# Performance work log

Hardware: AMD Instinct MI355X
Metric: run time of the kernel (lower is better)

The kernel has to match this reference:

```python
import jax, jax.numpy as jnp
import numpy as np

D_MODEL = 256; N_HEADS = 8; HEAD_DIM = 32; N_LEVELS = 4; N_POINTS = 4; N_LAYERS = 3; D_FFN = 1024
SHAPES = np.array([[76, 76], [38, 38], [19, 19], [10, 10]], dtype=np.int64)
S_TOTAL = int((SHAPES[:, 0] * SHAPES[:, 1]).sum())  # 7681


def setup_inputs():
    key = jax.random.key(0)
    ks = jax.random.split(key, 12)
    B = 1; C = D_MODEL; M = N_HEADS; Lv = N_LEVELS; P = N_POINTS; L = N_LAYERS; s = 0.02
    starts = np.concatenate([[0], np.cumsum(SHAPES[:, 0] * SHAPES[:, 1])[:-1]]).astype(np.int64)
    inp = {
        "src": jax.random.normal(ks[0], (B, S_TOTAL, C), jnp.float32),
        "pos": jax.random.normal(ks[1], (B, S_TOTAL, C), jnp.float32),
        "valid_ratios": jnp.ones((B, Lv, 2), jnp.float32),
        "spatial_shapes": jnp.asarray(SHAPES),
        "level_start_index": jnp.asarray(starts),
        "padding_mask": jnp.zeros((B, S_TOTAL), bool),
        "W_off": jax.random.normal(ks[2], (L, C, M * Lv * P * 2), jnp.float32) * s,
        "b_off": jax.random.normal(ks[3], (L, M * Lv * P * 2), jnp.float32) * s,
        "W_attn": jax.random.normal(ks[4], (L, C, M * Lv * P), jnp.float32) * s,
        "b_attn": jax.random.normal(ks[5], (L, M * Lv * P), jnp.float32) * s,
        "W_val": jax.random.normal(ks[6], (L, C, C), jnp.float32) * s,
        "b_val": jnp.zeros((L, C), jnp.float32),
        "W_out": jax.random.normal(ks[7], (L, C, C), jnp.float32) * s,
        "b_out": jnp.zeros((L, C), jnp.float32),
        "ln1_g": jnp.ones((L, C), jnp.float32),
        "ln1_b": jnp.zeros((L, C), jnp.float32),
        "W_ff1": jax.random.normal(ks[8], (L, C, D_FFN), jnp.float32) * s,
        "b_ff1": jnp.zeros((L, D_FFN), jnp.float32),
        "W_ff2": jax.random.normal(ks[9], (L, D_FFN, C), jnp.float32) * s,
        "b_ff2": jnp.zeros((L, C), jnp.float32),
        "ln2_g": jnp.ones((L, C), jnp.float32),
        "ln2_b": jnp.zeros((L, C), jnp.float32),
    }
    return inp


def _ln(x, g, b):
    mu = x.mean(-1, keepdims=True)
    var = ((x - mu) ** 2).mean(-1, keepdims=True)
    return (x - mu) * jax.lax.rsqrt(var + 1e-5) * g + b


def _gather(v, idx):
    # v: [B, HW, M, D], idx: [B, S, M, P] -> [B, S, M, P, D], head-specific gather
    B, S, M, P = idx.shape
    def one(vb, ib):
        i2 = ib.transpose(0, 2, 1).reshape(S * P, M, 1)
        o = jnp.take_along_axis(vb, i2, axis=0)  # [S*P, M, D]
        return o.reshape(S, P, M, -1).transpose(0, 2, 1, 3)
    return jax.vmap(one)(v, idx)


def _msda(query, src, mask, ref, shapes, starts, Wo, bo, Wa, ba, Wv, bv, Wout, bout):
    # Multi-scale deformable attention (Deformable-DETR), grid_sample align_corners=False + zero padding
    B, S, C = src.shape
    M, Lv, P, D = N_HEADS, N_LEVELS, N_POINTS, HEAD_DIM
    value = src @ Wv + bv
    value = jnp.where(mask[..., None], 0.0, value).reshape(B, S, M, D)
    off = (query @ Wo + bo).reshape(B, S, M, Lv, P, 2)
    aw = jax.nn.softmax((query @ Wa + ba).reshape(B, S, M, Lv * P), -1).reshape(B, S, M, Lv, P)
    norm = jnp.asarray(shapes[:, ::-1].copy(), jnp.float32)  # (W, H) per level
    loc = ref[:, :, None, :, None, :] + off / norm[None, None, None, :, None, :]  # [B,S,M,Lv,P,2]
    out = jnp.zeros((B, S, M, D), query.dtype)
    for lvl in range(Lv):
        H = int(shapes[lvl, 0]); W = int(shapes[lvl, 1]); st = int(starts[lvl])
        v = value[:, st:st + H * W]  # [B, H*W, M, D]
        l = loc[:, :, :, lvl]  # [B, S, M, P, 2]
        x = l[..., 0] * W - 0.5
        y = l[..., 1] * H - 0.5
        x0 = jnp.floor(x); y0 = jnp.floor(y)
        dx = x - x0; dy = y - y0
        samp = jnp.zeros((B, S, M, P, D), query.dtype)
        for yy, xx, w in ((y0, x0, (1 - dy) * (1 - dx)), (y0, x0 + 1, (1 - dy) * dx),
                          (y0 + 1, x0, dy * (1 - dx)), (y0 + 1, x0 + 1, dy * dx)):
            valid = (xx >= 0) & (xx < W) & (yy >= 0) & (yy < H)
            xi = jnp.clip(xx, 0, W - 1).astype(jnp.int32)
            yi = jnp.clip(yy, 0, H - 1).astype(jnp.int32)
            g = _gather(v, yi * W + xi)
            samp = samp + (w * valid)[..., None] * g
        out = out + (aw[:, :, :, lvl, :, None] * samp).sum(3)
    return out.reshape(B, S, C) @ Wout + bout


def _ref_points(vr, shapes):
    refs = []
    for lvl in range(shapes.shape[0]):
        H = int(shapes[lvl, 0]); W = int(shapes[lvl, 1])
        ry, rx = np.meshgrid(np.linspace(0.5, H - 0.5, H, dtype=np.float32),
                             np.linspace(0.5, W - 0.5, W, dtype=np.float32), indexing="ij")
        rxj = jnp.asarray(rx.reshape(-1))[None] / (vr[:, None, lvl, 0] * W)
        ryj = jnp.asarray(ry.reshape(-1))[None] / (vr[:, None, lvl, 1] * H)
        refs.append(jnp.stack([rxj, ryj], -1))
    ref = jnp.concatenate(refs, 1)  # [B, S, 2]
    return ref[:, :, None] * vr[:, None]  # [B, S, Lv, 2]


def _encoder(src, pos, valid_ratios, shapes, starts, mask, params):
    (W_off, b_off, W_attn, b_attn, W_val, b_val, W_out, b_out,
     ln1_g, ln1_b, W_ff1, b_ff1, W_ff2, b_ff2, ln2_g, ln2_b) = params
    ref = _ref_points(valid_ratios, shapes)
    out = src
    for l in range(N_LAYERS):
        q = out + pos  # with_pos_embed
        a = _msda(q, out, mask, ref, shapes, starts, W_off[l], b_off[l], W_attn[l], b_attn[l],
                  W_val[l], b_val[l], W_out[l], b_out[l])
        out = _ln(out + a, ln1_g[l], ln1_b[l])
        f = jax.nn.relu(out @ W_ff1[l] + b_ff1[l]) @ W_ff2[l] + b_ff2[l]
        out = _ln(out + f, ln2_g[l], ln2_b[l])
    return out


def reference(src, pos, valid_ratios, spatial_shapes, level_start_index, padding_mask,
              W_off, b_off, W_attn, b_attn, W_val, b_val, W_out, b_out,
              ln1_g, ln1_b, W_ff1, b_ff1, W_ff2, b_ff2, ln2_g, ln2_b):
    shapes = np.asarray(spatial_shapes)
    starts = np.asarray(level_start_index)
    params = (W_off, b_off, W_attn, b_attn, W_val, b_val, W_out, b_out,
              ln1_g, ln1_b, W_ff1, b_ff1, W_ff2, b_ff2, ln2_g, ln2_b)
    return _encoder(src, pos, valid_ratios, shapes, starts, padding_mask, params)
```

## Files before the change

kernel.cpp:

```cpp
#include <hip/hip_runtime.h>
#include <hip/hip_bf16.h>
#include <math.h>

#define S_TOTAL 7681

typedef __attribute__((ext_vector_type(8))) short bf16x8;
typedef __attribute__((ext_vector_type(4))) float f32x4;

__device__ __forceinline__ short f2b(float x) {
    union { float f; unsigned u; } v; v.f = x;
    unsigned r = v.u + 0x7FFFu + ((v.u >> 16) & 1u);
    return (short)(r >> 16);
}
__device__ __forceinline__ float b2f(unsigned short u) {
    union { unsigned u; float f; } t; t.u = ((unsigned)u) << 16; return t.f;
}

#define BM 128
#define BN 64
#define BK 32
#define KP 40

#define N4_TOT 491584
__global__ __launch_bounds__(256) void prologue_kernel(
    const float* __restrict__ s0, const float* __restrict__ s1,
    const float* __restrict__ s2, const float* __restrict__ s3,
    const float* __restrict__ s4, const float* __restrict__ s5,
    short* __restrict__ d0, short* __restrict__ d1, short* __restrict__ d2,
    short* __restrict__ d3, short* __restrict__ d4, short* __restrict__ d5,
    const float4* __restrict__ src, const float4* __restrict__ pos,
    float4* __restrict__ o, ushort4* __restrict__ xb, ushort4* __restrict__ qb)
{
    int b = blockIdx.x;
    if (b >= 2208) {
        int i = (b - 2208) * 256 + threadIdx.x;
        if (i < N4_TOT) {
            float4 v = src[i], p = pos[i];
            o[i] = v;
            ushort4 h, hq;
            h.x = (unsigned short)f2b(v.x); h.y = (unsigned short)f2b(v.y);
            h.z = (unsigned short)f2b(v.z); h.w = (unsigned short)f2b(v.w);
            hq.x = (unsigned short)f2b(v.x + p.x); hq.y = (unsigned short)f2b(v.y + p.y);
            hq.z = (unsigned short)f2b(v.z + p.z); hq.w = (unsigned short)f2b(v.w + p.w);
            xb[i] = h;
            qb[i] = hq;
        }
        return;
    }
    const int z = b / 736;
    int t = b - z * 736;
    const float* src_w; short* dst; int K, N, lt;
    if (t < 64)       { src_w = s0 + (size_t)z * 65536;  dst = d0 + (size_t)z * 65536;  K = 256;  N = 256;  lt = t; }
    else if (t < 128) { src_w = s1 + (size_t)z * 65536;  dst = d1 + (size_t)z * 98304;  K = 256;  N = 256;  lt = t - 64; }
    else if (t < 160) { src_w = s2 + (size_t)z * 32768;  dst = d2 + (size_t)z * 98304;  K = 256;  N = 128;  lt = t - 128; }
    else if (t < 224) { src_w = s3 + (size_t)z * 65536;  dst = d3 + (size_t)z * 65536;  K = 256;  N = 256;  lt = t - 160; }
    else if (t < 480) { src_w = s4 + (size_t)z * 262144; dst = d4 + (size_t)z * 262144; K = 256;  N = 1024; lt = t - 224; }
    else              { src_w = s5 + (size_t)z * 262144; dst = d5 + (size_t)z * 262144; K = 1024; N = 256;  lt = t - 480; }
    const int ntx = N >> 5;
    const int tk = (lt / ntx) << 5, tn = (lt % ntx) << 5;
    __shared__ float tile[32][33];
    const int cx = threadIdx.x & 31, cy = threadIdx.x >> 5;
    #pragma unroll
    for (int i = 0; i < 32; i += 8)
        tile[cy + i][cx] = src_w[(size_t)(tk + cy + i) * N + tn + cx];
    __syncthreads();
    #pragma unroll
    for (int i = 0; i < 32; i += 8)
        dst[(size_t)(tn + cy + i) * K + tk + cx] = f2b(tile[cx][cy + i]);
}

__global__ __launch_bounds__(256) void gemm_va_kernel(
    const short* __restrict__ xb, const short* __restrict__ qb,
    const short* __restrict__ Wt_val, const short* __restrict__ Wt_oa,
    const float* __restrict__ b_val, const float* __restrict__ b_off,
    const float* __restrict__ b_attn,
    short* __restrict__ value_bf, float* __restrict__ offbuf, int M)
{
    const int grp = (blockIdx.y >= 4);
    const short* A  = grp ? qb : xb;
    const short* Wt = grp ? Wt_oa : Wt_val;
    const int colBase = (grp ? (blockIdx.y - 4) : blockIdx.y) * BN;
    const int K = 256;

    __shared__ __align__(16) short As[BM * KP];
    __shared__ __align__(16) short Bs[BN * KP];
    const int tid = threadIdx.x;
    const int lane = tid & 63;
    const int wave = tid >> 6;
    const int rowBase = blockIdx.x * BM;

    const int ar = tid >> 1;
    const int ak = (tid & 1) * 16;
    const int br = tid >> 2;
    const int bk = (tid & 3) * 8;

    const int frow = lane & 15;
    const int fko  = (lane >> 4) * 8;
    const int wm = wave * 32;

    f32x4 acc[2][4] = {};

    const int aRow = rowBase + ar;
    const bool aOk = aRow < M;
    const short* Ap = A + (size_t)aRow * K + ak;
    const short* Bp = Wt + (size_t)(colBase + br) * K + bk;

    bf16x8 a0 = {}, a1 = {}, b0 = {};
    if (aOk) { a0 = *(const bf16x8*)Ap; a1 = *(const bf16x8*)(Ap + 8); }
    b0 = *(const bf16x8*)Bp;

    for (int k0 = 0; k0 < K; k0 += BK) {
        *(bf16x8*)&As[ar * KP + ak]     = a0;
        *(bf16x8*)&As[ar * KP + ak + 8] = a1;
        *(bf16x8*)&Bs[br * KP + bk]     = b0;
        __syncthreads();

        const int kn = k0 + BK;
        if (kn < K) {
            if (aOk) { a0 = *(const bf16x8*)(Ap + kn); a1 = *(const bf16x8*)(Ap + kn + 8); }
            b0 = *(const bf16x8*)(Bp + kn);
        }

        bf16x8 af0 = *(const bf16x8*)&As[(wm + frow) * KP + fko];
        bf16x8 af1 = *(const bf16x8*)&As[(wm + 16 + frow) * KP + fko];
        #pragma unroll
        for (int j = 0; j < 4; ++j) {
            bf16x8 bfj = *(const bf16x8*)&Bs[(j * 16 + frow) * KP + fko];
            acc[0][j] = __builtin_amdgcn_mfma_f32_16x16x32_bf16(af0, bfj, acc[0][j], 0, 0, 0);
            acc[1][j] = __builtin_amdgcn_mfma_f32_16x16x32_bf16(af1, bfj, acc[1][j], 0, 0, 0);
        }
        __syncthreads();
    }

    const int erow = (lane >> 4) * 4;
    const int ecol = lane & 15;
    #pragma unroll
    for (int mi = 0; mi < 2; ++mi) {
        #pragma unroll
        for (int j = 0; j < 4; ++j) {
            int col = colBase + j * 16 + ecol;
            float bias = grp ? (col < 256 ? b_off[col] : b_attn[col - 256]) : b_val[col];
            #pragma unroll
            for (int r = 0; r < 4; ++r) {
                int row = rowBase + wm + mi * 16 + erow + r;
                if (row < M) {
                    float v = acc[mi][j][r] + bias;
                    if (grp) offbuf[(size_t)row * 384 + col] = v;
                    else     value_bf[(size_t)row * 256 + col] = f2b(v);
                }
            }
        }
    }
}

__global__ __launch_bounds__(256) void gemm_ff1_kernel(
    const short* __restrict__ A, const short* __restrict__ Wt,
    const float* __restrict__ bias, short* __restrict__ Cv,
    int M, int N, int K)
{
    __shared__ __align__(16) short As[BM * KP];
    __shared__ __align__(16) short Bs[BN * KP];
    const int tid = threadIdx.x;
    const int lane = tid & 63;
    const int wave = tid >> 6;
    const int rowBase = blockIdx.x * BM;
    const int colBase = blockIdx.y * BN;

    const int ar = tid >> 1;
    const int ak = (tid & 1) * 16;
    const int br = tid >> 2;
    const int bk = (tid & 3) * 8;

    const int frow = lane & 15;
    const int fko  = (lane >> 4) * 8;
    const int wm = wave * 32;

    f32x4 acc[2][4] = {};

    const int aRow = rowBase + ar;
    const bool aOk = aRow < M;
    const short* Ap = A + (size_t)aRow * K + ak;
    const short* Bp = Wt + (size_t)(colBase + br) * K + bk;

    bf16x8 a0 = {}, a1 = {}, b0 = {};
    if (aOk) { a0 = *(const bf16x8*)Ap; a1 = *(const bf16x8*)(Ap + 8); }
    b0 = *(const bf16x8*)Bp;

    for (int k0 = 0; k0 < K; k0 += BK) {
        *(bf16x8*)&As[ar * KP + ak]     = a0;
        *(bf16x8*)&As[ar * KP + ak + 8] = a1;
        *(bf16x8*)&Bs[br * KP + bk]     = b0;
        __syncthreads();

        const int kn = k0 + BK;
        if (kn < K) {
            if (aOk) { a0 = *(const bf16x8*)(Ap + kn); a1 = *(const bf16x8*)(Ap + kn + 8); }
            b0 = *(const bf16x8*)(Bp + kn);
        }

        bf16x8 af0 = *(const bf16x8*)&As[(wm + frow) * KP + fko];
        bf16x8 af1 = *(const bf16x8*)&As[(wm + 16 + frow) * KP + fko];
        #pragma unroll
        for (int j = 0; j < 4; ++j) {
            bf16x8 bfj = *(const bf16x8*)&Bs[(j * 16 + frow) * KP + fko];
            acc[0][j] = __builtin_amdgcn_mfma_f32_16x16x32_bf16(af0, bfj, acc[0][j], 0, 0, 0);
            acc[1][j] = __builtin_amdgcn_mfma_f32_16x16x32_bf16(af1, bfj, acc[1][j], 0, 0, 0);
        }
        __syncthreads();
    }

    const int erow = (lane >> 4) * 4;
    const int ecol = lane & 15;
    #pragma unroll
    for (int mi = 0; mi < 2; ++mi) {
        #pragma unroll
        for (int j = 0; j < 4; ++j) {
            #pragma unroll
            for (int r = 0; r < 4; ++r) {
                int row = rowBase + wm + mi * 16 + erow + r;
                if (row < M) {
                    int col = colBase + j * 16 + ecol;
                    float v = fmaxf(acc[mi][j][r] + bias[col], 0.f);
                    Cv[(size_t)row * N + col] = f2b(v);
                }
            }
        }
    }
}

__global__ __launch_bounds__(256) void msda_outln_kernel(
    const short* __restrict__ value, const float* __restrict__ offb,
    const short* __restrict__ Wt_out, const float* __restrict__ bias,
    const float* __restrict__ g, const float* __restrict__ bln,
    float* __restrict__ out, short* __restrict__ xb, int M)
{
    __shared__ __align__(16) char scratch[36864];
    __shared__ __align__(16) short mt[16 * 264];
    __shared__ float rsum[16][4], rsq[16][4], smu[16], srs[16];
    float*   soff = (float*)scratch;
    ushort4* sIdx = (ushort4*)(scratch + 12288);
    float4*  sWgt = (float4*)(scratch + 20480);
    short*   Bs   = (short*)scratch;

    const int bid = blockIdx.x;
    const int sb = (bid < 480) ? ((bid & 7) * 60 + (bid >> 3)) : 480;
    const int q0 = sb * 16;
    const int tid = threadIdx.x;
    const int lane = tid & 63;
    const int wave = tid >> 6;

    for (int t = 0; t < 2; ++t) {
        const int qs = q0 + t * 8;
        {
            const float4* src4 = (const float4*)offb;
            float4* soff4 = (float4*)soff;
            #pragma unroll
            for (int i = tid; i < 768; i += 256) {
                int qi = i / 96, j = i - qi * 96;
                int q = min(qs + qi, S_TOTAL - 1);
                soff4[qi * 96 + j] = src4[(size_t)q * 96 + j];
            }
        }
        __syncthreads();

        if (tid < 64) {
            const int qi = tid >> 3, m = tid & 7;
            float* lg = &soff[qi * 384 + 256 + m * 16];
            float mx = -1e30f;
            #pragma unroll
            for (int k = 0; k < 16; ++k) mx = fmaxf(mx, lg[k]);
            float e[16], sum = 0.f;
            #pragma unroll
            for (int k = 0; k < 16; ++k) { e[k] = expf(lg[k] - mx); sum += e[k]; }
            float inv = 1.f / sum;
            #pragma unroll
            for (int k = 0; k < 16; ++k) lg[k] = e[k] * inv;
        }
        __syncthreads();

        #pragma unroll
        for (int it = tid; it < 1024; it += 256) {
            const int qi = it >> 7, i = it & 127;
            const int lvl = (i >> 2) & 3;
            const int q = min(qs + qi, S_TOTAL - 1);

            float refx, refy;
            if (q < 5776)      { int u = q;        int r = u / 76, c = u % 76; refx = (c + 0.5f) / 76.f; refy = (r + 0.5f) / 76.f; }
            else if (q < 7220) { int u = q - 5776; int r = u / 38, c = u % 38; refx = (c + 0.5f) / 38.f; refy = (r + 0.5f) / 38.f; }
            else if (q < 7581) { int u = q - 7220; int r = u / 19, c = u % 19; refx = (c + 0.5f) / 19.f; refy = (r + 0.5f) / 19.f; }
            else               { int u = q - 7581; int r = u / 10, c = u % 10; refx = (c + 0.5f) / 10.f; refy = (r + 0.5f) / 10.f; }

            const int LVL_HW[4] = {76, 38, 19, 10};
            const int LVL_ST[4] = {0, 5776, 7220, 7581};
            const int W = LVL_HW[lvl];
            const float fW = (float)W;

            float ox = soff[qi * 384 + i * 2];
            float oy = soff[qi * 384 + i * 2 + 1];
            float aw = soff[qi * 384 + 256 + i];

            float x = refx * fW + ox - 0.5f;
            float y = refy * fW + oy - 0.5f;
            float x0f = floorf(x), y0f = floorf(y);
            int x0 = (int)x0f, y0 = (int)y0f;
            float dx = x - x0f, dy = y - y0f;

            bool vx0 = (x0 >= 0) & (x0 < W);
            bool vx1 = (x0 >= -1) & (x0 < W - 1);
            bool vy0 = (y0 >= 0) & (y0 < W);
            bool vy1 = (y0 >= -1) & (y0 < W - 1);
            int xc0 = min(max(x0, 0), W - 1), xc1 = min(max(x0 + 1, 0), W - 1);
            int yc0 = min(max(y0, 0), W - 1), yc1 = min(max(y0 + 1, 0), W - 1);
            int base = LVL_ST[lvl];
            ushort4 id;
            id.x = (unsigned short)(base + yc0 * W + xc0);
            id.y = (unsigned short)(base + yc0 * W + xc1);
            id.z = (unsigned short)(base + yc1 * W + xc0);
            id.w = (unsigned short)(base + yc1 * W + xc1);
            float4 w4;
            w4.x = (vy0 && vx0) ? (1.f - dy) * (1.f - dx) * aw : 0.f;
            w4.y = (vy0 && vx1) ? (1.f - dy) * dx * aw : 0.f;
            w4.z = (vy1 && vx0) ? dy * (1.f - dx) * aw : 0.f;
            w4.w = (vy1 && vx1) ? dy * dx * aw : 0.f;
            sIdx[it] = id;
            sWgt[it] = w4;
        }
        __syncthreads();

        {
            const int qi = wave * 2 + ((lane >> 5) & 1);
            const int l32 = lane & 31;
            const int h = l32 >> 2, dg = l32 & 3;
            const short* vcol = value + h * 32 + dg * 8;
            const int itb = qi * 128 + (h << 4);

            float a[8] = {};
            #pragma unroll
            for (int pt = 0; pt < 16; ++pt) {
                const ushort4 id = sIdx[itb + pt];
                const float4 w = sWgt[itb + pt];
                bf16x8 v0 = *(const bf16x8*)(vcol + ((size_t)id.x << 8));
                bf16x8 v1 = *(const bf16x8*)(vcol + ((size_t)id.y << 8));
                bf16x8 v2 = *(const bf16x8*)(vcol + ((size_t)id.z << 8));
                bf16x8 v3 = *(const bf16x8*)(vcol + ((size_t)id.w << 8));
                #pragma unroll
                for (int e = 0; e < 8; ++e)
                    a[e] += w.x * b2f((unsigned short)v0[e]) + w.y * b2f((unsigned short)v1[e])
                          + w.z * b2f((unsigned short)v2[e]) + w.w * b2f((unsigned short)v3[e]);
            }
            bf16x8 o;
            #pragma unroll
            for (int e = 0; e < 8; ++e) o[e] = f2b(a[e]);
            *(bf16x8*)&mt[(t * 8 + qi) * 264 + h * 32 + dg * 8] = o;
        }
        __syncthreads();
    }

    const int frow = lane & 15;
    const int fko  = (lane >> 4) * 8;

    f32x4 acc[4] = {};
    const short* Bp = Wt_out + (size_t)tid * 256;
    bf16x8 w0 = *(const bf16x8*)(Bp);      bf16x8 w1 = *(const bf16x8*)(Bp + 8);
    bf16x8 w2 = *(const bf16x8*)(Bp + 16); bf16x8 w3 = *(const bf16x8*)(Bp + 24);

    for (int k0 = 0; k0 < 256; k0 += BK) {
        *(bf16x8*)&Bs[tid * KP + 0]  = w0;
        *(bf16x8*)&Bs[tid * KP + 8]  = w1;
        *(bf16x8*)&Bs[tid * KP + 16] = w2;
        *(bf16x8*)&Bs[tid * KP + 24] = w3;
        __syncthreads();

        const int kn = k0 + BK;
        if (kn < 256) {
            w0 = *(const bf16x8*)(Bp + kn);      w1 = *(const bf16x8*)(Bp + kn + 8);
            w2 = *(const bf16x8*)(Bp + kn + 16); w3 = *(const bf16x8*)(Bp + kn + 24);
        }

        bf16x8 af = *(const bf16x8*)&mt[frow * 264 + k0 + fko];
        #pragma unroll
        for (int j = 0; j < 4; ++j) {
            bf16x8 bfj = *(const bf16x8*)&Bs[(wave * 64 + j * 16 + frow) * KP + fko];
            acc[j] = __builtin_amdgcn_mfma_f32_16x16x32_bf16(af, bfj, acc[j], 0, 0, 0);
        }
        __syncthreads();
    }

    const int erow = (lane >> 4) * 4;
    const int ecol = lane & 15;
    float x[4][4];
    #pragma unroll
    for (int j = 0; j < 4; ++j)
        #pragma unroll
        for (int r = 0; r < 4; ++r) {
            int row = q0 + erow + r;
            int col = wave * 64 + j * 16 + ecol;
            float res = (row < M) ? out[(size_t)row * 256 + col] : 0.f;
            x[j][r] = acc[j][r] + bias[col] + res;
        }

    #pragma unroll
    for (int r = 0; r < 4; ++r) {
        float s1 = x[0][r] + x[1][r] + x[2][r] + x[3][r];
        float s2 = x[0][r]*x[0][r] + x[1][r]*x[1][r] + x[2][r]*x[2][r] + x[3][r]*x[3][r];
        #pragma unroll
        for (int o = 1; o < 16; o <<= 1) {
            s1 += __shfl_xor(s1, o);
            s2 += __shfl_xor(s2, o);
        }
        if ((lane & 15) == 0) {
            rsum[erow + r][wave] = s1;
            rsq [erow + r][wave] = s2;
        }
    }
    __syncthreads();
    if (tid < 16) {
        float S1 = rsum[tid][0] + rsum[tid][1] + rsum[tid][2] + rsum[tid][3];
        float S2 = rsq[tid][0] + rsq[tid][1] + rsq[tid][2] + rsq[tid][3];
        float mu = S1 * (1.f / 256.f);
        smu[tid] = mu;
        srs[tid] = rsqrtf(S2 * (1.f / 256.f) - mu * mu + 1e-5f);
    }
    __syncthreads();

    #pragma unroll
    for (int r = 0; r < 4; ++r) {
        int lrow = erow + r;
        int row = q0 + lrow;
        if (row >= M) continue;
        float mu = smu[lrow], rs = srs[lrow];
        #pragma unroll
        for (int j = 0; j < 4; ++j) {
            int col = wave * 64 + j * 16 + ecol;
            float y = (x[j][r] - mu) * rs * g[col] + bln[col];
            out[(size_t)row * 256 + col] = y;
            xb[(size_t)row * 256 + col] = f2b(y);
        }
    }
}

template<int WRITEQ>
__global__ __launch_bounds__(256) void gemm_ln16_kernel(
    const short* __restrict__ A, const short* __restrict__ Wt,
    const float* __restrict__ bias, const float* __restrict__ g,
    const float* __restrict__ bln, const float* __restrict__ pos,
    float* __restrict__ out, short* __restrict__ xb, short* __restrict__ qb,
    int M, int K)
{
    __shared__ __align__(16) short As[16 * KP];
    __shared__ __align__(16) short Bs[256 * KP];
    __shared__ float rsum[16][4], rsq[16][4], smu[16], srs[16];

    const int tid = threadIdx.x;
    const int lane = tid & 63;
    const int wave = tid >> 6;
    const int rowBase = blockIdx.x * 16;

    const int frow = lane & 15;
    const int fko  = (lane >> 4) * 8;

    f32x4 acc[4] = {};

    const int ar = tid >> 1;
    const int ak = (tid & 1) * 16;
    const int aRow = rowBase + ar;
    const bool aOk = (tid < 32) && (aRow < M);
    const short* Ap = A + (size_t)aRow * K + ak;
    const short* Bp = Wt + (size_t)tid * K;

    bf16x8 a0 = {}, a1 = {};
    if (aOk) { a0 = *(const bf16x8*)Ap; a1 = *(const bf16x8*)(Ap + 8); }
    bf16x8 w0 = *(const bf16x8*)(Bp);      bf16x8 w1 = *(const bf16x8*)(Bp + 8);
    bf16x8 w2 = *(const bf16x8*)(Bp + 16); bf16x8 w3 = *(const bf16x8*)(Bp + 24);

    for (int k0 = 0; k0 < K; k0 += BK) {
        if (tid < 32) {
            *(bf16x8*)&As[ar * KP + ak]     = a0;
            *(bf16x8*)&As[ar * KP + ak + 8] = a1;
        }
        *(bf16x8*)&Bs[tid * KP + 0]  = w0;
        *(bf16x8*)&Bs[tid * KP + 8]  = w1;
        *(bf16x8*)&Bs[tid * KP + 16] = w2;
        *(bf16x8*)&Bs[tid * KP + 24] = w3;
        __syncthreads();

        const int kn = k0 + BK;
        if (kn < K) {
            if (aOk) { a0 = *(const bf16x8*)(Ap + kn); a1 = *(const bf16x8*)(Ap + kn + 8); }
            w0 = *(const bf16x8*)(Bp + kn);      w1 = *(const bf16x8*)(Bp + kn + 8);
            w2 = *(const bf16x8*)(Bp + kn + 16); w3 = *(const bf16x8*)(Bp + kn + 24);
        }

        bf16x8 af = *(const bf16x8*)&As[frow * KP + fko];
        #pragma unroll
        for (int j = 0; j < 4; ++j) {
            bf16x8 bfj = *(const bf16x8*)&Bs[(wave * 64 + j * 16 + frow) * KP + fko];
            acc[j] = __builtin_amdgcn_mfma_f32_16x16x32_bf16(af, bfj, acc[j], 0, 0, 0);
        }
        __syncthreads();
    }

    const int erow = (lane >> 4) * 4;
    const int ecol = lane & 15;
    float x[4][4];
    #pragma unroll
    for (int j = 0; j < 4; ++j)
        #pragma unroll
        for (int r = 0; r < 4; ++r) {
            int row = rowBase + erow + r;
            int col = wave * 64 + j * 16 + ecol;
            float res = (row < M) ? out[(size_t)row * 256 + col] : 0.f;
            x[j][r] = acc[j][r] + bias[col] + res;
        }

    #pragma unroll
    for (int r = 0; r < 4; ++r) {
        float s1 = x[0][r] + x[1][r] + x[2][r] + x[3][r];
        float s2 = x[0][r]*x[0][r] + x[1][r]*x[1][r] + x[2][r]*x[2][r] + x[3][r]*x[3][r];
        #pragma unroll
        for (int o = 1; o < 16; o <<= 1) {
            s1 += __shfl_xor(s1, o);
            s2 += __shfl_xor(s2, o);
        }
        if ((lane & 15) == 0) {
            rsum[erow + r][wave] = s1;
            rsq [erow + r][wave] = s2;
        }
    }
    __syncthreads();
    if (tid < 16) {
        float S1 = rsum[tid][0] + rsum[tid][1] + rsum[tid][2] + rsum[tid][3];
        float S2 = rsq[tid][0] + rsq[tid][1] + rsq[tid][2] + rsq[tid][3];
        float mu = S1 * (1.f / 256.f);
        smu[tid] = mu;
        srs[tid] = rsqrtf(S2 * (1.f / 256.f) - mu * mu + 1e-5f);
    }
    __syncthreads();

    #pragma unroll
    for (int r = 0; r < 4; ++r) {
        int lrow = erow + r;
        int row = rowBase + lrow;
        if (row >= M) continue;
        float mu = smu[lrow], rs = srs[lrow];
        #pragma unroll
        for (int j = 0; j < 4; ++j) {
            int col = wave * 64 + j * 16 + ecol;
            float y = (x[j][r] - mu) * rs * g[col] + bln[col];
            out[(size_t)row * 256 + col] = y;
            xb[(size_t)row * 256 + col] = f2b(y);
            if (WRITEQ)
                qb[(size_t)row * 256 + col] = f2b(y + pos[(size_t)row * 256 + col]);
        }
    }
}

extern "C" void kernel_launch(void* const* d_in, const int* in_sizes, int n_in,
                              void* d_out, int out_size, void* d_ws, size_t ws_size,
                              hipStream_t stream) {
    const float* src    = (const float*)d_in[0];
    const float* pos    = (const float*)d_in[1];
    const float* W_off  = (const float*)d_in[6];
    const float* b_off  = (const float*)d_in[7];
    const float* W_attn = (const float*)d_in[8];
    const float* b_attn = (const float*)d_in[9];
    const float* W_val  = (const float*)d_in[10];
    const float* b_val  = (const float*)d_in[11];
    const float* W_out  = (const float*)d_in[12];
    const float* b_out  = (const float*)d_in[13];
    const float* ln1_g  = (const float*)d_in[14];
    const float* ln1_b  = (const float*)d_in[15];
    const float* W_ff1  = (const float*)d_in[16];
    const float* b_ff1  = (const float*)d_in[17];
    const float* W_ff2  = (const float*)d_in[18];
    const float* b_ff2  = (const float*)d_in[19];
    const float* ln2_g  = (const float*)d_in[20];
    const float* ln2_b  = (const float*)d_in[21];

    const size_t S = S_TOTAL;
    float* out = (float*)d_out;

    short* wt = (short*)d_ws;
    short* Wt_val = wt;
    short* Wt_oa  = wt + 196608;
    short* Wt_out = wt + 491520;
    short* Wt_ff1 = wt + 688128;
    short* Wt_ff2 = wt + 1474560;
    float* fbase  = (float*)d_ws + 1131648;
    short* xb       = (short*)fbase;
    short* qb       = (short*)(fbase + 128 * S);
    short* value_bf = (short*)(fbase + 256 * S);
    float* offb     = fbase + 384 * S;
    short* hid      = (short*)(fbase + 256 * S);

    prologue_kernel<<<4129, 256, 0, stream>>>(
        W_val, W_off, W_attn, W_out, W_ff1, W_ff2,
        Wt_val, Wt_oa, Wt_oa + 65536, Wt_out, Wt_ff1, Wt_ff2,
        (const float4*)src, (const float4*)pos,
        (float4*)out, (ushort4*)xb, (ushort4*)qb);

    const int MB = (S_TOTAL + BM - 1) / BM;
    const int LB = (S_TOTAL + 15) / 16;

    for (int l = 0; l < 3; ++l) {
        gemm_va_kernel<<<dim3(MB, 10), 256, 0, stream>>>(
            xb, qb, Wt_val + (size_t)l * 65536, Wt_oa + (size_t)l * 98304,
            b_val + (size_t)l * 256, b_off + (size_t)l * 256, b_attn + (size_t)l * 128,
            value_bf, offb, S_TOTAL);
        msda_outln_kernel<<<LB, 256, 0, stream>>>(
            value_bf, offb, Wt_out + (size_t)l * 65536, b_out + (size_t)l * 256,
            ln1_g + (size_t)l * 256, ln1_b + (size_t)l * 256,
            out, xb, S_TOTAL);
        gemm_ff1_kernel<<<dim3(MB, 16), 256, 0, stream>>>(
            xb, Wt_ff1 + (size_t)l * 262144, b_ff1 + (size_t)l * 1024, hid,
            S_TOTAL, 1024, 256);
        gemm_ln16_kernel<1><<<LB, 256, 0, stream>>>(
            hid, Wt_ff2 + (size_t)l * 262144, b_ff2 + (size_t)l * 256,
            ln2_g + (size_t)l * 256, ln2_b + (size_t)l * 256, pos,
            out, xb, qb, S_TOTAL, 1024);
    }
}
```

Measured before the change: 449.1 us.

## Split MSDA sampling from output projection and reuse the LN GEMM kernel

The fused MSDA+out-proj+LayerNorm kernel is split into two. A standalone sampling kernel processes 8 queries per block over 968 blocks and writes bf16 results to a new global buffer. The existing gemm_ln16 kernel (WRITEQ=0) then does the output projection, residual add and LayerNorm. This is meant to raise block count and occupancy for the gather-heavy sampling stage and to use the tuned GEMM path. In exchange it adds a kernel launch and a global round trip of the sampled activations.

```diff
diff --git a/kernel.cpp b/kernel.cpp
--- a/kernel.cpp
+++ b/kernel.cpp
@@ -228,215 +228,129 @@
     }
 }
 
-__global__ __launch_bounds__(256) void msda_outln_kernel(
+__global__ __launch_bounds__(256) void msda_kernel(
     const short* __restrict__ value, const float* __restrict__ offb,
-    const short* __restrict__ Wt_out, const float* __restrict__ bias,
-    const float* __restrict__ g, const float* __restrict__ bln,
-    float* __restrict__ out, short* __restrict__ xb, int M)
+    short* __restrict__ msdab)
 {
-    __shared__ __align__(16) char scratch[36864];
-    __shared__ __align__(16) short mt[16 * 264];
-    __shared__ float rsum[16][4], rsq[16][4], smu[16], srs[16];
+    __shared__ __align__(16) char scratch[24576];
     float*   soff = (float*)scratch;
-    ushort4* sIdx = (ushort4*)(scratch + 12288);
-    float4*  sWgt = (float4*)(scratch + 20480);
-    short*   Bs   = (short*)scratch;
+    ushort4* sIdx = (ushort4*)scratch;
+    float4*  sWgt = (float4*)(scratch + 8192);
 
     const int bid = blockIdx.x;
-    const int sb = (bid < 480) ? ((bid & 7) * 60 + (bid >> 3)) : 480;
-    const int q0 = sb * 16;
+    const int sb = (bid & 7) * 121 + (bid >> 3);
+    const int q0 = sb * 8;
+    if (q0 >= S_TOTAL) return;
     const int tid = threadIdx.x;
+
+    {
+        const float4* src4 = (const float4*)offb;
+        float4* soff4 = (float4*)soff;
+        #pragma unroll
+        for (int i = tid; i < 768; i += 256) {
+            int qi = i / 96, j = i - qi * 96;
+            int q = min(q0 + qi, S_TOTAL - 1);
+            soff4[qi * 96 + j] = src4[(size_t)q * 96 + j];
+        }
+    }
+    __syncthreads();
+
+    if (tid < 64) {
+        const int qi = tid >> 3, m = tid & 7;
+        float* lg = &soff[qi * 384 + 256 + m * 16];
+        float mx = -1e30f;
+        #pragma unroll
+        for (int k = 0; k < 16; ++k) mx = fmaxf(mx, lg[k]);
+        float e[16], sum = 0.f;
+        #pragma unroll
+        for (int k = 0; k < 16; ++k) { e[k] = expf(lg[k] - mx); sum += e[k]; }
+        float inv = 1.f / sum;
+        #pragma unroll
+        for (int k = 0; k < 16; ++k) lg[k] = e[k] * inv;
+    }
+    __syncthreads();
+
+    ushort4 rid[4];
+    float4  rw[4];
+    #pragma unroll
+    for (int k = 0; k < 4; ++k) {
+        const int it = tid + k * 256;
+        const int qi = it >> 7, i = it & 127;
+        const int lvl = (i >> 2) & 3;
+        const int q = min(q0 + qi, S_TOTAL - 1);
+
+        float refx, refy;
+        if (q < 5776)      { int u = q;        int r = u / 76, c = u % 76; refx = (c + 0.5f) / 76.f; refy = (r + 0.5f) / 76.f; }
+        else if (q < 7220) { int u = q - 5776; int r = u / 38, c = u % 38; refx = (c + 0.5f) / 38.f; refy = (r + 0.5f) / 38.f; }
+        else if (q < 7581) { int u = q - 7220; int r = u / 19, c = u % 19; refx = (c + 0.5f) / 19.f; refy = (r + 0.5f) / 19.f; }
+        else               { int u = q - 7581; int r = u / 10, c = u % 10; refx = (c + 0.5f) / 10.f; refy = (r + 0.5f) / 10.f; }
+
+        const int LVL_HW[4] = {76, 38, 19, 10};
+        const int LVL_ST[4] = {0, 5776, 7220, 7581};
+        const int W = LVL_HW[lvl];
+        const float fW = (float)W;
+
+        float ox = soff[qi * 384 + i * 2];
+        float oy = soff[qi * 384 + i * 2 + 1];
+        float aw = soff[qi * 384 + 256 + i];
+
+        float x = refx * fW + ox - 0.5f;
+        float y = refy * fW + oy - 0.5f;
+        float x0f = floorf(x), y0f = floorf(y);
+        int x0 = (int)x0f, y0 = (int)y0f;
+        float dx = x - x0f, dy = y - y0f;
+
+        bool vx0 = (x0 >= 0) & (x0 < W);
+        bool vx1 = (x0 >= -1) & (x0 < W - 1);
+        bool vy0 = (y0 >= 0) & (y0 < W);
+        bool vy1 = (y0 >= -1) & (y0 < W - 1);
+        int xc0 = min(max(x0, 0), W - 1), xc1 = min(max(x0 + 1, 0), W - 1);
+        int yc0 = min(max(y0, 0), W - 1), yc1 = min(max(y0 + 1, 0), W - 1);
+        int base = LVL_ST[lvl];
+        rid[k].x = (unsigned short)(base + yc0 * W + xc0);
+        rid[k].y = (unsigned short)(base + yc0 * W + xc1);
+        rid[k].z = (unsigned short)(base + yc1 * W + xc0);
+        rid[k].w = (unsigned short)(base + yc1 * W + xc1);
+        rw[k].x = (vy0 && vx0) ? (1.f - dy) * (1.f - dx) * aw : 0.f;
+        rw[k].y = (vy0 && vx1) ? (1.f - dy) * dx * aw : 0.f;
+        rw[k].z = (vy1 && vx0) ? dy * (1.f - dx) * aw : 0.f;
+        rw[k].w = (vy1 && vx1) ? dy * dx * aw : 0.f;
+    }
+    __syncthreads();
+    #pragma unroll
+    for (int k = 0; k < 4; ++k) {
+        sIdx[tid + k * 256] = rid[k];
+        sWgt[tid + k * 256] = rw[k];
+    }
+    __syncthreads();
+
     const int lane = tid & 63;
-    const int wave = tid >> 6;
-
-    for (int t = 0; t < 2; ++t) {
-        const int qs = q0 + t * 8;
-        {
-            const float4* src4 = (const float4*)offb;
-            float4* soff4 = (float4*)soff;
-            #pragma unroll
-            for (int i = tid; i < 768; i += 256) {
-                int qi = i / 96, j = i - qi * 96;
-                int q = min(qs + qi, S_TOTAL - 1);
-                soff4[qi * 96 + j] = src4[(size_t)q * 96 + j];
-            }
-        }
-        __syncthreads();
-
-        if (tid < 64) {
-            const int qi = tid >> 3, m = tid & 7;
-            float* lg = &soff[qi * 384 + 256 + m * 16];
-            float mx = -1e30f;
-            #pragma unroll
-            for (int k = 0; k < 16; ++k) mx = fmaxf(mx, lg[k]);
-            float e[16], sum = 0.f;
-            #pragma unroll
-            for (int k = 0; k < 16; ++k) { e[k] = expf(lg[k] - mx); sum += e[k]; }
-            float inv = 1.f / sum;
-            #pragma unroll
-            for (int k = 0; k < 16; ++k) lg[k] = e[k] * inv;
-        }
-        __syncthreads();
-
-        #pragma unroll
-        for (int it = tid; it < 1024; it += 256) {
-            const int qi = it >> 7, i = it & 127;
-            const int lvl = (i >> 2) & 3;
-            const int q = min(qs + qi, S_TOTAL - 1);
-
-            float refx, refy;
-            if (q < 5776)      { int u = q;        int r = u / 76, c = u % 76; refx = (c + 0.5f) / 76.f; refy = (r + 0.5f) / 76.f; }
-            else if (q < 7220) { int u = q - 5776; int r = u / 38, c = u % 38; refx = (c + 0.5f) / 38.f; refy = (r + 0.5f) / 38.f; }
-            else if (q < 7581) { int u = q - 7220; int r = u / 19, c = u % 19; refx = (c + 0.5f) / 19.f; refy = (r + 0.5f) / 19.f; }
-            else               { int u = q - 7581; int r = u / 10, c = u % 10; refx = (c + 0.5f) / 10.f; refy = (r + 0.5f) / 10.f; }
-
-            const int LVL_HW[4] = {76, 38, 19, 10};
-            const int LVL_ST[4] = {0, 5776, 7220, 7581};
-            const int W = LVL_HW[lvl];
-            const float fW = (float)W;
-
-            float ox = soff[qi * 384 + i * 2];
-            float oy = soff[qi * 384 + i * 2 + 1];
-            float aw = soff[qi * 384 + 256 + i];
-
-            float x = refx * fW + ox - 0.5f;
-            float y = refy * fW + oy - 0.5f;
-            float x0f = floorf(x), y0f = floorf(y);
-            int x0 = (int)x0f, y0 = (int)y0f;
-            float dx = x - x0f, dy = y - y0f;
-
-            bool vx0 = (x0 >= 0) & (x0 < W);
-            bool vx1 = (x0 >= -1) & (x0 < W - 1);
-            bool vy0 = (y0 >= 0) & (y0 < W);
-            bool vy1 = (y0 >= -1) & (y0 < W - 1);
-            int xc0 = min(max(x0, 0), W - 1), xc1 = min(max(x0 + 1, 0), W - 1);
-            int yc0 = min(max(y0, 0), W - 1), yc1 = min(max(y0 + 1, 0), W - 1);
-            int base = LVL_ST[lvl];
-            ushort4 id;
-            id.x = (unsigned short)(base + yc0 * W + xc0);
-            id.y = (unsigned short)(base + yc0 * W + xc1);
-            id.z = (unsigned short)(base + yc1 * W + xc0);
-            id.w = (unsigned short)(base + yc1 * W + xc1);
-            float4 w4;
-            w4.x = (vy0 && vx0) ? (1.f - dy) * (1.f - dx) * aw : 0.f;
-            w4.y = (vy0 && vx1) ? (1.f - dy) * dx * aw : 0.f;
-            w4.z = (vy1 && vx0) ? dy * (1.f - dx) * aw : 0.f;
-            w4.w = (vy1 && vx1) ? dy * dx * aw : 0.f;
-            sIdx[it] = id;
-            sWgt[it] = w4;
-        }
-        __syncthreads();
-
-        {
-            const int qi = wave * 2 + ((lane >> 5) & 1);
-            const int l32 = lane & 31;
-            const int h = l32 >> 2, dg = l32 & 3;
-            const short* vcol = value + h * 32 + dg * 8;
-            const int itb = qi * 128 + (h << 4);
-
-            float a[8] = {};
-            #pragma unroll
-            for (int pt = 0; pt < 16; ++pt) {
-                const ushort4 id = sIdx[itb + pt];
-                const float4 w = sWgt[itb + pt];
-                bf16x8 v0 = *(const bf16x8*)(vcol + ((size_t)id.x << 8));
-                bf16x8 v1 = *(const bf16x8*)(vcol + ((size_t)id.y << 8));
-                bf16x8 v2 = *(const bf16x8*)(vcol + ((size_t)id.z << 8));
-                bf16x8 v3 = *(const bf16x8*)(vcol + ((size_t)id.w << 8));
-                #pragma unroll
-                for (int e = 0; e < 8; ++e)
-                    a[e] += w.x * b2f((unsigned short)v0[e]) + w.y * b2f((unsigned short)v1[e])
-                          + w.z * b2f((unsigned short)v2[e]) + w.w * b2f((unsigned short)v3[e]);
-            }
-            bf16x8 o;
-            #pragma unroll
-            for (int e = 0; e < 8; ++e) o[e] = f2b(a[e]);
-            *(bf16x8*)&mt[(t * 8 + qi) * 264 + h * 32 + dg * 8] = o;
-        }
-        __syncthreads();
-    }
-
-    const int frow = lane & 15;
-    const int fko  = (lane >> 4) * 8;
-
-    f32x4 acc[4] = {};
-    const short* Bp = Wt_out + (size_t)tid * 256;
-    bf16x8 w0 = *(const bf16x8*)(Bp);      bf16x8 w1 = *(const bf16x8*)(Bp + 8);
-    bf16x8 w2 = *(const bf16x8*)(Bp + 16); bf16x8 w3 = *(const bf16x8*)(Bp + 24);
-
-    for (int k0 = 0; k0 < 256; k0 += BK) {
-        *(bf16x8*)&Bs[tid * KP + 0]  = w0;
-        *(bf16x8*)&Bs[tid * KP + 8]  = w1;
-        *(bf16x8*)&Bs[tid * KP + 16] = w2;
-        *(bf16x8*)&Bs[tid * KP + 24] = w3;
-        __syncthreads();
-
-        const int kn = k0 + BK;
-        if (kn < 256) {
-            w0 = *(const bf16x8*)(Bp + kn);      w1 = *(const bf16x8*)(Bp + kn + 8);
-            w2 = *(const bf16x8*)(Bp + kn + 16); w3 = *(const bf16x8*)(Bp + kn + 24);
-        }
-
-        bf16x8 af = *(const bf16x8*)&mt[frow * 264 + k0 + fko];
-        #pragma unroll
-        for (int j = 0; j < 4; ++j) {
-            bf16x8 bfj = *(const bf16x8*)&Bs[(wave * 64 + j * 16 + frow) * KP + fko];
-            acc[j] = __builtin_amdgcn_mfma_f32_16x16x32_bf16(af, bfj, acc[j], 0, 0, 0);
-        }
-        __syncthreads();
-    }
-
-    const int erow = (lane >> 4) * 4;
-    const int ecol = lane & 15;
-    float x[4][4];
-    #pragma unroll
-    for (int j = 0; j < 4; ++j)
-        #pragma unroll
-        for (int r = 0; r < 4; ++r) {
-            int row = q0 + erow + r;
-            int col = wave * 64 + j * 16 + ecol;
-            float res = (row < M) ? out[(size_t)row * 256 + col] : 0.f;
-            x[j][r] = acc[j][r] + bias[col] + res;
-        }
-
-    #pragma unroll
-    for (int r = 0; r < 4; ++r) {
-        float s1 = x[0][r] + x[1][r] + x[2][r] + x[3][r];
-        float s2 = x[0][r]*x[0][r] + x[1][r]*x[1][r] + x[2][r]*x[2][r] + x[3][r]*x[3][r];
-        #pragma unroll
-        for (int o = 1; o < 16; o <<= 1) {
-            s1 += __shfl_xor(s1, o);
-            s2 += __shfl_xor(s2, o);
-        }
-        if ((lane & 15) == 0) {
-            rsum[erow + r][wave] = s1;
-            rsq [erow + r][wave] = s2;
-        }
-    }
-    __syncthreads();
-    if (tid < 16) {
-        float S1 = rsum[tid][0] + rsum[tid][1] + rsum[tid][2] + rsum[tid][3];
-        float S2 = rsq[tid][0] + rsq[tid][1] + rsq[tid][2] + rsq[tid][3];
-        float mu = S1 * (1.f / 256.f);
-        smu[tid] = mu;
-        srs[tid] = rsqrtf(S2 * (1.f / 256.f) - mu * mu + 1e-5f);
-    }
-    __syncthreads();
-
-    #pragma unroll
-    for (int r = 0; r < 4; ++r) {
-        int lrow = erow + r;
-        int row = q0 + lrow;
-        if (row >= M) continue;
-        float mu = smu[lrow], rs = srs[lrow];
-        #pragma unroll
-        for (int j = 0; j < 4; ++j) {
-            int col = wave * 64 + j * 16 + ecol;
-            float y = (x[j][r] - mu) * rs * g[col] + bln[col];
-            out[(size_t)row * 256 + col] = y;
-            xb[(size_t)row * 256 + col] = f2b(y);
-        }
-    }
+    const int qi = (tid >> 6) * 2 + (lane >> 5);
+    const int q = q0 + qi;
+    if (q >= S_TOTAL) return;
+    const int l32 = lane & 31;
+    const int h = l32 >> 2, dg = l32 & 3;
+    const short* vcol = value + h * 32 + dg * 8;
+    const int itb = qi * 128 + (h << 4);
+
+    float a[8] = {};
+    #pragma unroll
+    for (int pt = 0; pt < 16; ++pt) {
+        const ushort4 id = sIdx[itb + pt];
+        const float4 w = sWgt[itb + pt];
+        bf16x8 v0 = *(const bf16x8*)(vcol + ((size_t)id.x << 8));
+        bf16x8 v1 = *(const bf16x8*)(vcol + ((size_t)id.y << 8));
+        bf16x8 v2 = *(const bf16x8*)(vcol + ((size_t)id.z << 8));
+        bf16x8 v3 = *(const bf16x8*)(vcol + ((size_t)id.w << 8));
+        #pragma unroll
+        for (int e = 0; e < 8; ++e)
+            a[e] += w.x * b2f((unsigned short)v0[e]) + w.y * b2f((unsigned short)v1[e])
+                  + w.z * b2f((unsigned short)v2[e]) + w.w * b2f((unsigned short)v3[e]);
+    }
+    bf16x8 o;
+    #pragma unroll
+    for (int e = 0; e < 8; ++e) o[e] = f2b(a[e]);
+    *(bf16x8*)(msdab + (size_t)q * 256 + h * 32 + dg * 8) = o;
 }
 
 template<int WRITEQ>
@@ -591,6 +505,7 @@
     short* qb       = (short*)(fbase + 128 * S);
     short* value_bf = (short*)(fbase + 256 * S);
     float* offb     = fbase + 384 * S;
+    short* msdab    = (short*)(fbase + 768 * S);
     short* hid      = (short*)(fbase + 256 * S);
 
     prologue_kernel<<<4129, 256, 0, stream>>>(
@@ -607,10 +522,11 @@
             xb, qb, Wt_val + (size_t)l * 65536, Wt_oa + (size_t)l * 98304,
             b_val + (size_t)l * 256, b_off + (size_t)l * 256, b_attn + (size_t)l * 128,
             value_bf, offb, S_TOTAL);
-        msda_outln_kernel<<<LB, 256, 0, stream>>>(
-            value_bf, offb, Wt_out + (size_t)l * 65536, b_out + (size_t)l * 256,
-            ln1_g + (size_t)l * 256, ln1_b + (size_t)l * 256,
-            out, xb, S_TOTAL);
+        msda_kernel<<<968, 256, 0, stream>>>(value_bf, offb, msdab);
+        gemm_ln16_kernel<0><<<LB, 256, 0, stream>>>(
+            msdab, Wt_out + (size_t)l * 65536, b_out + (size_t)l * 256,
+            ln1_g + (size_t)l * 256, ln1_b + (size_t)l * 256, pos,
+            out, xb, qb, S_TOTAL, 256);
         gemm_ff1_kernel<<<dim3(MB, 16), 256, 0, stream>>>(
             xb, Wt_ff1 + (size_t)l * 262144, b_ff1 + (size_t)l * 1024, hid,
             S_TOTAL, 1024, 256);
```

Result: no change. 451.4 us (+0.5%).
